# Optimization experiments

Measured on AMD Instinct MI355X. Metric: run time of the kernel, lower is better.

The kernel has to match this reference:

```python
import jax, jax.numpy as jnp
import numpy as np
from jax import lax

TAU = 2.0  # SynapseFilter time constant (learnable=False)


def setup_inputs() -> dict:
    key = jax.random.key(0)
    T, N, C, D_out = 64, 16, 128, 256
    k1, k2 = jax.random.split(key)
    x = jax.random.uniform(k1, (T, N, C, 2), dtype=jnp.float32)  # spike-like input (T,N,C,2)
    # matches torch init: _log_delay = log(linspace(1e-7, 1, D_out)).view(-1,1)
    log_delay = jnp.log(jnp.linspace(1e-7, 1.0, D_out, dtype=jnp.float32)).reshape(D_out, 1)
    log_weight = jnp.log(jnp.float32(2.0))
    # uniform noise replacing torch.bernoulli(p) (u < p  <=>  bernoulli(p))
    noise = jax.random.uniform(k2, (N, C, D_out, 2), dtype=jnp.float32)
    return {"x": x, "log_delay": log_delay, "log_weight": log_weight, "noise": noise}


def reference(x, log_delay, log_weight, noise):
    T, N, C, _ = x.shape
    D_out = log_delay.shape[0]

    # delay property: cat([exp(log_delay), flip(exp(log_delay))], dim=1) -> (D_out, 2)
    d = jnp.exp(log_delay)                      # (D_out, 1)
    delay = jnp.concatenate([d, d[::-1]], axis=1)  # (D_out, 2)

    # stochastic rounding of T * delay, broadcast to (N, C, D_out, 2)
    scaled = jnp.broadcast_to((T * delay)[None, None], (N, C, D_out, 2))
    fl = jnp.floor(scaled)
    rounded = fl + (noise < (scaled - fl)).astype(scaled.dtype)

    # clamp(max = T - 1 - argmax over time). argmax of the repeated tensor equals
    # argmax of x broadcast over D_out, so compute it cheaply on x.
    am = jnp.argmax(x, axis=0)                  # (N, C, 2)
    max_d = (T - 1 - am)[:, :, None, :]         # (N, C, 1, 2)
    rd = jnp.minimum(rounded.astype(jnp.int32), max_d.astype(jnp.int32))  # (N,C,D_out,2)

    # circular delay-line shift: out[t] = in[(t - delay) mod T]
    out_rep = jnp.broadcast_to(x[:, :, :, None, :], (T, N, C, D_out, 2))
    t_idx = jnp.arange(T, dtype=jnp.int32)[:, None, None, None, None]
    idx = (t_idx - rd[None]) % T                # (T, N, C, D_out, 2)
    shifted = jnp.take_along_axis(out_rep, idx, axis=0)

    # SynapseFilter (multi-step): y_t = y_{t-1} * (1 - 1/tau) + x_t, y_{-1}=0
    decay = jnp.float32(1.0 - 1.0 / TAU)

    def step(carry, xt):
        carry = carry * decay + xt
        return carry, carry

    _, y = lax.scan(step, jnp.zeros_like(shifted[0]), shifted)  # (T,N,C,D_out,2)

    # scale by weight = exp(log_weight), sum over D_in=2
    out = (y * jnp.exp(log_weight)).sum(axis=-1)  # (T, N, C, D_out)
    return out
```

## Files before the change

kernel.cpp:

```cpp
#include <hip/hip_runtime.h>
#include <math.h>

#define T_STEPS 64
#define D_OUT 256

__global__ __launch_bounds__(256) void jeffress_kernel(
    const float* __restrict__ x,
    const float* __restrict__ log_delay,
    const float* __restrict__ log_weight,
    const float* __restrict__ noise,
    float* __restrict__ out,
    int NC)
{
    __shared__ float xs0[T_STEPS];
    __shared__ float xs1[T_STEPS];
    __shared__ int maxd[2];

    const int nc = blockIdx.x;
    const int j  = threadIdx.x;

    if (j < T_STEPS) {
        const float* xp = x + ((size_t)j * NC + nc) * 2;
        xs0[j] = xp[0];
        xs1[j] = xp[1];
    }
    __syncthreads();

    if (j < 2) {
        const float* xsrc = (j == 0) ? xs0 : xs1;
        float best = xsrc[0];
        int bi = 0;
        for (int t = 1; t < T_STEPS; ++t) {
            float v = xsrc[t];
            if (v > best) { best = v; bi = t; }
        }
        maxd[j] = (T_STEPS - 1) - bi;
    }
    __syncthreads();

    double ld0 = (double)log_delay[j];
    double ld1 = (double)log_delay[(D_OUT - 1) - j];
    double s0 = (double)T_STEPS * exp(ld0);
    double s1 = (double)T_STEPS * exp(ld1);
    double f0 = floor(s0), f1 = floor(s1);

    const float* nptr = noise + ((size_t)nc * D_OUT + j) * 2;
    float n0 = nptr[0], n1 = nptr[1];

    int r0 = (int)f0 + (((double)n0 < (s0 - f0)) ? 1 : 0);
    int r1 = (int)f1 + (((double)n1 < (s1 - f1)) ? 1 : 0);
    int rd0 = min(r0, maxd[0]);
    int rd1 = min(r1, maxd[1]);

    const float w = (float)exp((double)log_weight[0]);

    float y0 = 0.f, y1 = 0.f;
    float* op = out + (size_t)nc * D_OUT + j;
    const size_t ostride = (size_t)NC * D_OUT;
    #pragma unroll
    for (int t = 0; t < T_STEPS; ++t) {
        y0 = y0 * 0.5f + xs0[(t - rd0) & (T_STEPS - 1)];
        y1 = y1 * 0.5f + xs1[(t - rd1) & (T_STEPS - 1)];
        op[(size_t)t * ostride] = (y0 + y1) * w;
    }
}

extern "C" void kernel_launch(void* const* d_in, const int* in_sizes, int n_in,
                              void* d_out, int out_size, void* d_ws, size_t ws_size,
                              hipStream_t stream) {
    const float* x          = (const float*)d_in[0];
    const float* log_delay  = (const float*)d_in[1];
    const float* log_weight = (const float*)d_in[2];
    const float* noise      = (const float*)d_in[3];
    float* out = (float*)d_out;

    const int NC = in_sizes[3] / (D_OUT * 2);

    jeffress_kernel<<<NC, D_OUT, 0, stream>>>(x, log_delay, log_weight, noise, out, NC);
}
```

Before: 147.5 us.

## Use one wavefront per block with four outputs per thread and shuffle argmax

Each block now runs as a single 64-lane wavefront, and every thread computes four consecutive D_out columns. Results are written as float4 stores, and log_delay and noise are read with float4 vector loads. The serial two-thread argmax and its block barrier are replaced by a wavefront xor-shuffle reduction with first-index tie-breaking. This cuts serial argmax latency and the number of memory instructions. The cost is fewer resident threads for hiding latency and more per-thread register state.

```diff
diff --git a/kernel.cpp b/kernel.cpp
--- a/kernel.cpp
+++ b/kernel.cpp
@@ -4,7 +4,7 @@
 #define T_STEPS 64
 #define D_OUT 256
 
-__global__ __launch_bounds__(256) void jeffress_kernel(
+__global__ __launch_bounds__(64) void jeffress_kernel(
     const float* __restrict__ x,
     const float* __restrict__ log_delay,
     const float* __restrict__ log_weight,
@@ -14,54 +14,70 @@
 {
     __shared__ float xs0[T_STEPS];
     __shared__ float xs1[T_STEPS];
-    __shared__ int maxd[2];
 
     const int nc = blockIdx.x;
-    const int j  = threadIdx.x;
+    const int l  = threadIdx.x;
+    const int j0 = l << 2;
 
-    if (j < T_STEPS) {
-        const float* xp = x + ((size_t)j * NC + nc) * 2;
-        xs0[j] = xp[0];
-        xs1[j] = xp[1];
+    const float2 xv = *(const float2*)(x + ((size_t)l * NC + nc) * 2);
+    xs0[l] = xv.x;
+    xs1[l] = xv.y;
+
+    float v0 = xv.x, v1 = xv.y;
+    int   i0 = l,    i1 = l;
+    #pragma unroll
+    for (int off = 1; off < 64; off <<= 1) {
+        float ov0 = __shfl_xor(v0, off);
+        int   oi0 = __shfl_xor(i0, off);
+        float ov1 = __shfl_xor(v1, off);
+        int   oi1 = __shfl_xor(i1, off);
+        if (ov0 > v0 || (ov0 == v0 && oi0 < i0)) { v0 = ov0; i0 = oi0; }
+        if (ov1 > v1 || (ov1 == v1 && oi1 < i1)) { v1 = ov1; i1 = oi1; }
     }
-    __syncthreads();
+    const int maxd0 = (T_STEPS - 1) - i0;
+    const int maxd1 = (T_STEPS - 1) - i1;
 
-    if (j < 2) {
-        const float* xsrc = (j == 0) ? xs0 : xs1;
-        float best = xsrc[0];
-        int bi = 0;
-        for (int t = 1; t < T_STEPS; ++t) {
-            float v = xsrc[t];
-            if (v > best) { best = v; bi = t; }
-        }
-        maxd[j] = (T_STEPS - 1) - bi;
+    const float4 ldf = *(const float4*)(log_delay + j0);
+    const float4 ldr = *(const float4*)(log_delay + (D_OUT - 4 - j0));
+    const float4 nA  = *(const float4*)(noise + ((size_t)nc * D_OUT + j0) * 2);
+    const float4 nB  = *(const float4*)(noise + ((size_t)nc * D_OUT + j0) * 2 + 4);
+
+    const float ld0[4] = { ldf.x, ldf.y, ldf.z, ldf.w };
+    const float ld1[4] = { ldr.w, ldr.z, ldr.y, ldr.x };
+    const float n0[4]  = { nA.x, nA.z, nB.x, nB.z };
+    const float n1[4]  = { nA.y, nA.w, nB.y, nB.w };
+
+    int rd0[4], rd1[4];
+    #pragma unroll
+    for (int k = 0; k < 4; ++k) {
+        double s0 = (double)T_STEPS * exp((double)ld0[k]);
+        double s1 = (double)T_STEPS * exp((double)ld1[k]);
+        double f0 = floor(s0), f1 = floor(s1);
+        int r0 = (int)f0 + (((double)n0[k] < (s0 - f0)) ? 1 : 0);
+        int r1 = (int)f1 + (((double)n1[k] < (s1 - f1)) ? 1 : 0);
+        rd0[k] = min(r0, maxd0);
+        rd1[k] = min(r1, maxd1);
     }
-    __syncthreads();
-
-    double ld0 = (double)log_delay[j];
-    double ld1 = (double)log_delay[(D_OUT - 1) - j];
-    double s0 = (double)T_STEPS * exp(ld0);
-    double s1 = (double)T_STEPS * exp(ld1);
-    double f0 = floor(s0), f1 = floor(s1);
-
-    const float* nptr = noise + ((size_t)nc * D_OUT + j) * 2;
-    float n0 = nptr[0], n1 = nptr[1];
-
-    int r0 = (int)f0 + (((double)n0 < (s0 - f0)) ? 1 : 0);
-    int r1 = (int)f1 + (((double)n1 < (s1 - f1)) ? 1 : 0);
-    int rd0 = min(r0, maxd[0]);
-    int rd1 = min(r1, maxd[1]);
 
     const float w = (float)exp((double)log_weight[0]);
 
-    float y0 = 0.f, y1 = 0.f;
-    float* op = out + (size_t)nc * D_OUT + j;
+    __syncthreads();
+
+    float y0[4] = {0.f, 0.f, 0.f, 0.f};
+    float y1[4] = {0.f, 0.f, 0.f, 0.f};
+    float* op = out + (size_t)nc * D_OUT + j0;
     const size_t ostride = (size_t)NC * D_OUT;
+
     #pragma unroll
     for (int t = 0; t < T_STEPS; ++t) {
-        y0 = y0 * 0.5f + xs0[(t - rd0) & (T_STEPS - 1)];
-        y1 = y1 * 0.5f + xs1[(t - rd1) & (T_STEPS - 1)];
-        op[(size_t)t * ostride] = (y0 + y1) * w;
+        float4 o;
+        #pragma unroll
+        for (int k = 0; k < 4; ++k) {
+            y0[k] = y0[k] * 0.5f + xs0[(t - rd0[k]) & (T_STEPS - 1)];
+            y1[k] = y1[k] * 0.5f + xs1[(t - rd1[k]) & (T_STEPS - 1)];
+            (&o.x)[k] = (y0[k] + y1[k]) * w;
+        }
+        *(float4*)(op + (size_t)t * ostride) = o;
     }
 }
 
@@ -76,5 +92,5 @@
 
     const int NC = in_sizes[3] / (D_OUT * 2);
 
-    jeffress_kernel<<<NC, D_OUT, 0, stream>>>(x, log_delay, log_weight, noise, out, NC);
+    jeffress_kernel<<<NC, T_STEPS, 0, stream>>>(x, log_delay, log_weight, noise, out, NC);
 }
```

Result: no change. 145.8 us (-1.2%).
